# Optimization experiments

Hardware: AMD Instinct MI355X
Metric: run time of the kernel (lower is better)

## Reference

```python
import jax, jax.numpy as jnp
import numpy as np

LN_EPS = 1e-5


def _layer_norm(h, g, b):
    mu = jnp.mean(h, axis=-1, keepdims=True)
    var = jnp.mean((h - mu) ** 2, axis=-1, keepdims=True)
    return (h - mu) / jnp.sqrt(var + LN_EPS) * g + b


def setup_inputs() -> dict:
    key = jax.random.key(0)
    ks = jax.random.split(key, 12)
    B, N, D = 2, 2048, 768
    H, Dh = 12, 64
    Dp = D // 4  # 192, DynamicPositionBias width
    s = lambda fan_in: 1.0 / np.sqrt(fan_in)
    return {
        "x": jax.random.normal(ks[0], (B, N, D), jnp.float32),
        "qkv_w": jax.random.normal(ks[1], (D, 3 * H * Dh), jnp.float32) * s(D),
        "qkv_b": jax.random.normal(ks[2], (3 * H * Dh,), jnp.float32) * 0.02,
        "out_w": jax.random.normal(ks[3], (H * Dh, D), jnp.float32) * s(H * Dh),
        "out_b": jax.random.normal(ks[4], (D,), jnp.float32) * 0.02,
        "dpb_w_in": jax.random.normal(ks[5], (1, Dp), jnp.float32),
        "dpb_b_in": jax.random.normal(ks[6], (Dp,), jnp.float32) * 0.02,
        "dpb_w_hid": jax.random.normal(ks[7], (3, Dp, Dp), jnp.float32) * s(Dp),
        "dpb_b_hid": jax.random.normal(ks[8], (3, Dp), jnp.float32) * 0.02,
        "dpb_ln_g": jnp.ones((4, Dp), jnp.float32),
        "dpb_ln_b": jnp.zeros((4, Dp), jnp.float32),
        "dpb_w_out": jax.random.normal(ks[9], (Dp, 12), jnp.float32) * s(Dp),
        "dpb_b_out": jax.random.normal(ks[10], (12,), jnp.float32) * 0.02,
    }


def _dpb_bias(n, w_in, b_in, w_hid, b_hid, ln_g, ln_b, w_out, b_out):
    # positions -n+1 .. n-1, log-distance transform
    pos = jnp.arange(-n + 1, n, dtype=jnp.float32)[:, None]  # [2n-1, 1]
    pos = jnp.sign(pos) * jnp.log(jnp.abs(pos) + 1.0)
    h = jax.nn.silu(_layer_norm(pos @ w_in + b_in, ln_g[0], ln_b[0]))
    for l in range(3):
        h = jax.nn.silu(_layer_norm(h @ w_hid[l] + b_hid[l], ln_g[l + 1], ln_b[l + 1]))
    vals = h @ w_out + b_out  # [2n-1, H]
    idx = jnp.arange(n)[:, None] - jnp.arange(n)[None, :] + (n - 1)  # [n, n]
    bias = vals[idx]  # [n, n, H]
    return jnp.transpose(bias, (2, 0, 1))  # [H, n, n]


def reference(x, qkv_w, qkv_b, out_w, out_b,
              dpb_w_in, dpb_b_in, dpb_w_hid, dpb_b_hid,
              dpb_ln_g, dpb_ln_b, dpb_w_out, dpb_b_out):
    B, N, D = x.shape
    H = dpb_w_out.shape[-1]
    qkv = x @ qkv_w + qkv_b  # [B, N, 3*H*Dh]
    q, k, v = jnp.split(qkv, 3, axis=-1)
    split_heads = lambda t: jnp.transpose(t.reshape(B, N, H, -1), (0, 2, 1, 3))
    q, k, v = split_heads(q), split_heads(k), split_heads(v)  # [B, H, N, Dh]
    Dh = q.shape[-1]

    bias = _dpb_bias(N, dpb_w_in, dpb_b_in, dpb_w_hid, dpb_b_hid,
                     dpb_ln_g, dpb_ln_b, dpb_w_out, dpb_b_out)  # [H, N, N]

    scale = Dh ** -0.5
    sim = jnp.einsum("bhid,bhjd->bhij", q, k) * scale + bias[None]
    attn = jax.nn.softmax(sim, axis=-1)
    o = jnp.einsum("bhij,bhjd->bhid", attn, v)  # [B, H, N, Dh]
    o = jnp.transpose(o, (0, 2, 1, 3)).reshape(B, N, H * Dh)
    return o @ out_w + out_b
```

## Files before the change

### kernel.cpp

```cpp
#include <hip/hip_runtime.h>
#include <stdint.h>
#include <stddef.h>

typedef __bf16 bf16;
typedef __bf16 bf16x8 __attribute__((ext_vector_type(8)));
typedef float floatx4 __attribute__((ext_vector_type(4)));

typedef __attribute__((address_space(1))) void as1_void;
typedef __attribute__((address_space(3))) void as3_void;

__device__ __forceinline__ void async_ld16(const void* g, void* l) {
    __builtin_amdgcn_global_load_lds((as1_void*)g, (as3_void*)l, 16, 0, 0);
}

__device__ __forceinline__ floatx4 mfma16(bf16x8 a, bf16x8 b, floatx4 c) {
    return __builtin_amdgcn_mfma_f32_16x16x32_bf16(a, b, c, 0, 0, 0);
}

__device__ __forceinline__ unsigned cvtpk_bf16(float lo, float hi) {
    unsigned r;
    asm("v_cvt_pk_bf16_f32 %0, %1, %2" : "=v"(r) : "v"(lo), "v"(hi));
    return r;
}
__device__ __forceinline__ void pl32swap(unsigned &a, unsigned &b) {
    asm("v_permlane32_swap_b32 %0, %1" : "+v"(a), "+v"(b));
}
__device__ __forceinline__ void pl16swap(unsigned &a, unsigned &b) {
    asm("v_permlane16_swap_b32 %0, %1" : "+v"(a), "+v"(b));
}

#define LOG2E 1.4426950408889634f
#define SM_M2 24.0f
#define DP 192

__device__ __forceinline__ float ldsc(const void* p, size_t i, int isbf) {
    return isbf ? (float)((const bf16*)p)[i] : ((const float*)p)[i];
}
__device__ __forceinline__ bf16x8 ld8(const void* p, size_t i, int isbf) {
    if (isbf) return *(const bf16x8*)((const bf16*)p + i);
    const float* f = (const float*)p + i;
    float4 lo = *(const float4*)(f);
    float4 hi = *(const float4*)(f + 4);
    bf16x8 r;
    r[0]=(bf16)lo.x; r[1]=(bf16)lo.y; r[2]=(bf16)lo.z; r[3]=(bf16)lo.w;
    r[4]=(bf16)hi.x; r[5]=(bf16)hi.y; r[6]=(bf16)hi.z; r[7]=(bf16)hi.w;
    return r;
}
__device__ __forceinline__ int get_fl(const uint32_t* lng) {
    return (lng[0] == 0x3F803F80u) ? 1 : 0;
}

__device__ void transpose_body(const void* in, bf16* out, int R, int C,
                               int bx, int by, int fl, bf16 (*tile)[65]) {
    int c0 = bx * 64, r0 = by * 64;
    for (int i = threadIdx.x; i < 64*64; i += 256) {
        int rr = i >> 6, cc = i & 63;
        int gr = r0 + rr, gc = c0 + cc;
        tile[rr][cc] = (gr < R && gc < C)
                       ? (bf16)ldsc(in, (size_t)gr * C + gc, fl) : (bf16)0.0f;
    }
    __syncthreads();
    for (int i = threadIdx.x; i < 64*64; i += 256) {
        int rr = i >> 6, cc = i & 63;
        int oR = c0 + rr, oC = r0 + cc;
        if (oR < C && oC < R) out[(size_t)oR * R + oC] = tile[cc][rr];
    }
}

__global__ __launch_bounds__(256) void prep_kernel(
    const void* __restrict__ qkv_w, const void* __restrict__ out_w,
    bf16* __restrict__ wt_qkv, bf16* __restrict__ wt_out,
    const void* __restrict__ w_hid, const void* __restrict__ w_out,
    bf16* __restrict__ WtH, bf16* __restrict__ Wt12,
    const uint32_t* __restrict__ lngw,
    const void* __restrict__ x, bf16* __restrict__ xbf)
{
    __shared__ bf16 tile[64][65];
    const int fl = get_fl(lngw);
    const int bid = blockIdx.x;
    if (bid < 432) {
        transpose_body(qkv_w, wt_qkv, 768, 2304, bid % 36, bid / 36, fl, tile);
        return;
    }
    if (bid < 576) {
        int b2 = bid - 432;
        transpose_body(out_w, wt_out, 768, 768, b2 % 12, b2 / 12, fl, tile);
        return;
    }
    if (bid < 603) {
        transpose_body((const char*)0 + 0, nullptr, 0, 0, 0, 0, fl, tile);
        return;
    }
    if (bid < 606) {
        transpose_body(w_out, Wt12, 192, 12, 0, bid - 603, fl, tile);
        return;
    }
    size_t base = (size_t)(bid - 606) * 6144 + threadIdx.x * 8;
    #pragma unroll
    for (int c = 0; c < 3; c++)
        *(bf16x8*)(xbf + base + c*2048) = ld8(x, base + c*2048, fl);
}

__global__ __launch_bounds__(256) void prep_whid_kernel(
    const void* __restrict__ w_hid, bf16* __restrict__ WtH,
    const uint32_t* __restrict__ lngw)
{
    __shared__ bf16 tile[64][65];
    const int fl = get_fl(lngw);
    int l = blockIdx.x / 9, t9 = blockIdx.x % 9;
    transpose_body((const char*)w_hid + 0 + (size_t)l * DP * DP * (fl ? 2 : 4),
                   WtH + (size_t)l * DP * DP, DP, DP, t9 % 3, t9 / 3, fl, tile);
}

#define GK 768
#define HS 200

__global__ __launch_bounds__(256) void gemm0_dpb_kernel(
    const bf16* __restrict__ A, const bf16* __restrict__ Bt,
    const void* __restrict__ bias, const uint32_t* __restrict__ lngw,
    bf16* __restrict__ out0, bf16* __restrict__ out1, bf16* __restrict__ out2,
    const void* __restrict__ w_in, const void* __restrict__ b_in,
    const void* __restrict__ b_hid, const void* __restrict__ ln_g,
    const void* __restrict__ ln_b, const void* __restrict__ b_out,
    const bf16* __restrict__ WtH, const bf16* __restrict__ Wt12,
    float* __restrict__ vals_t)
{
    __shared__ __align__(16) char smem[16896];
    const int fl = get_fl(lngw);
    const int tid = threadIdx.x;
    const int wave = tid >> 6, lane = tid & 63;
    const int g = lane >> 4, cl = lane & 15;

    if (blockIdx.x >= 576) {
        bf16*  Hb   = (bf16*)smem;
        float* redS = (float*)(smem + 6400);
        float* redQ = (float*)(smem + 6656);
        const int pbase = (blockIdx.x - 576) * 16;

        float tpos[4];
        #pragma unroll
        for (int rg = 0; rg < 4; rg++) {
            int p = pbase + g*4 + rg;
            float pv = (float)p - 2047.0f;
            float sg = (pv > 0.0f) ? 1.0f : ((pv < 0.0f) ? -1.0f : 0.0f);
            tpos[rg] = sg * logf(fabsf(pv) + 1.0f);
        }
        int col[3];
        #pragma unroll
        for (int tt = 0; tt < 3; tt++) col[tt] = (wave*3 + tt)*16 + cl;

        floatx4 acc[3];
        #pragma unroll
        for (int tt = 0; tt < 3; tt++) {
            float wi = ldsc(w_in, col[tt], fl), bi = ldsc(b_in, col[tt], fl);
            #pragma unroll
            for (int rg = 0; rg < 4; rg++) acc[tt][rg] = tpos[rg]*wi + bi;
        }

        #pragma unroll 1
        for (int l = 0; l < 4; l++) {
            float s1[4], s2[4];
            #pragma unroll
            for (int rg = 0; rg < 4; rg++) {
                s1[rg] = acc[0][rg] + acc[1][rg] + acc[2][rg];
                s2[rg] = acc[0][rg]*acc[0][rg] + acc[1][rg]*acc[1][rg]
                       + acc[2][rg]*acc[2][rg];
            }
            #pragma unroll
            for (int m = 1; m <= 8; m <<= 1)
                #pragma unroll
                for (int rg = 0; rg < 4; rg++) {
                    s1[rg] += __shfl_xor(s1[rg], m);
                    s2[rg] += __shfl_xor(s2[rg], m);
                }
            if (cl == 0)
                #pragma unroll
                for (int rg = 0; rg < 4; rg++) {
                    redS[wave*16 + g*4 + rg] = s1[rg];
                    redQ[wave*16 + g*4 + rg] = s2[rg];
                }
            __syncthreads();
            float mu[4], rstd[4];
            #pragma unroll
            for (int rg = 0; rg < 4; rg++) {
                int row = g*4 + rg;
                float S = redS[row] + redS[16+row] + redS[32+row] + redS[48+row];
                float Q = redQ[row] + redQ[16+row] + redQ[32+row] + redQ[48+row];
                float m_ = S * (1.0f/DP);
                float v_ = Q * (1.0f/DP) - m_*m_;
                mu[rg] = m_;
                rstd[rg] = 1.0f / sqrtf(v_ + 1e-5f);
            }
            #pragma unroll
            for (int tt = 0; tt < 3; tt++) {
                float ga = ldsc(ln_g, l*DP + col[tt], fl);
                float be = ldsc(ln_b, l*DP + col[tt], fl);
                #pragma unroll
                for (int rg = 0; rg < 4; rg++) {
                    float y = (acc[tt][rg] - mu[rg]) * rstd[rg] * ga + be;
                    float sil = y / (1.0f + __expf(-y));
                    Hb[(g*4 + rg)*HS + col[tt]] = (bf16)sil;
                }
            }
            __syncthreads();
            if (l == 3) break;
            #pragma unroll
            for (int tt = 0; tt < 3; tt++) {
                float bh = ldsc(b_hid, l*DP + col[tt], fl);
                #pragma unroll
                for (int rg = 0; rg < 4; rg++) acc[tt][rg] = bh;
            }
            const bf16* Wl = WtH + (size_t)l * DP * DP;
            #pragma unroll
            for (int ks = 0; ks < 6; ks++) {
                bf16x8 af = *(const bf16x8*)(Hb + cl*HS + ks*32 + g*8);
                #pragma unroll
                for (int tt = 0; tt < 3; tt++) {
                    bf16x8 bfv = *(const bf16x8*)(Wl + (size_t)col[tt]*DP
                                                  + ks*32 + g*8);
                    acc[tt] = mfma16(af, bfv, acc[tt]);
                }
            }
        }
        if (wave == 0) {
            floatx4 facc = {};
            if (cl < 12) {
                float bo = ldsc(b_out, cl, fl);
                #pragma unroll
                for (int rg = 0; rg < 4; rg++) facc[rg] = bo;
            }
            #pragma unroll
            for (int ks = 0; ks < 6; ks++) {
                bf16x8 af = *(const bf16x8*)(Hb + cl*HS + ks*32 + g*8);
                bf16x8 bfv = {};
                if (cl < 12)
                    bfv = *(const bf16x8*)(Wt12 + (size_t)cl*DP + ks*32 + g*8);
                facc = mfma16(af, bfv, facc);
            }
            if (cl < 12)
                #pragma unroll
                for (int rg = 0; rg < 4; rg++) {
                    int p = pbase + g*4 + rg;
                    if (p < 4095) vals_t[cl*4095 + p] = facc[rg];
                }
        }
        return;
    }

    bf16* As = (bf16*)smem;
    bf16* Bs = (bf16*)(smem + 8192);
    const int tile = blockIdx.x;
    const int m0 = (tile / 18) * 128, n0 = (tile % 18) * 128;
    const int wm = (wave >> 1) * 64, wn = (wave & 1) * 64;

    const int e0 = wave*512 + lane*8;
    const int e1 = e0 + 2048;
    const int r0 = e0 >> 5, c0e = e0 & 31;
    const int r1 = e1 >> 5, c1e = e1 & 31;
    const bf16* Ag0 = A  + (size_t)(m0 + r0) * GK + c0e;
    const bf16* Ag1 = A  + (size_t)(m0 + r1) * GK + c1e;
    const bf16* Bg0 = Bt + (size_t)(n0 + r0) * GK + c0e;
    const bf16* Bg1 = Bt + (size_t)(n0 + r1) * GK + c1e;
    bf16* Al0 = As + e0;
    bf16* Al1 = As + e1;
    bf16* Bl0 = Bs + e0;
    bf16* Bl1 = Bs + e1;

    const int frow = lane & 15, fk = (lane >> 4) * 8;
    floatx4 acc[4][4] = {};

    for (int k0 = 0; k0 < GK; k0 += 32) {
        __syncthreads();
        async_ld16(Ag0 + k0, Al0);
        async_ld16(Ag1 + k0, Al1);
        async_ld16(Bg0 + k0, Bl0);
        async_ld16(Bg1 + k0, Bl1);
        __syncthreads();
        bf16x8 af[4], bfr[4];
        #pragma unroll
        for (int i = 0; i < 4; i++)
            af[i] = *(const bf16x8*)(As + (wm + i*16 + frow)*32 + fk);
        #pragma unroll
        for (int j = 0; j < 4; j++)
            bfr[j] = *(const bf16x8*)(Bs + (wn + j*16 + frow)*32 + fk);
        #pragma unroll
        for (int i = 0; i < 4; i++)
            #pragma unroll
            for (int j = 0; j < 4; j++)
                acc[i][j] = mfma16(af[i], bfr[j], acc[i][j]);
    }

    #pragma unroll
    for (int i = 0; i < 4; i++) {
        #pragma unroll
        for (int j = 0; j < 4; j++) {
            int Cc = n0 + wn + j*16 + cl;
            float bv = ldsc(bias, Cc, fl);
            #pragma unroll
            for (int rg = 0; rg < 4; rg++) {
                int R = m0 + wm + i*16 + g*4 + rg;
                float val = acc[i][j][rg] + bv;
                int which = Cc / 768;
                int c2 = Cc - which * 768;
                int hh = c2 >> 6, dd = c2 & 63;
                int bb = R >> 11, nn = R & 2047;
                if (which == 2) {
                    out2[(((size_t)(bb*12 + hh) * 64 + dd) * 2048) + nn]
                        = (bf16)val;
                } else {
                    bf16* dst = (which == 0) ? out0 : out1;
                    dst[((size_t)(bb*12 + hh) * 2048 + nn) * 64 + dd] = (bf16)val;
                }
            }
        }
    }
}

__global__ __launch_bounds__(256) void gemm_out(
    const bf16* __restrict__ A, const bf16* __restrict__ Bt,
    const void* __restrict__ bias, const uint32_t* __restrict__ lngw,
    void* __restrict__ out0)
{
    __shared__ __align__(16) bf16 As[128*32];
    __shared__ __align__(16) bf16 Bs[128*32];
    const int fl  = get_fl(lngw);
    const int tid = threadIdx.x;
    const int wave = tid >> 6, lane = tid & 63;
    const int m0 = blockIdx.y * 128, n0 = blockIdx.x * 128;
    const int wm = (wave >> 1) * 64, wn = (wave & 1) * 64;

    const int e0 = wave*512 + lane*8;
    const int e1 = e0 + 2048;
    const int r0 = e0 >> 5, c0e = e0 & 31;
    const int r1 = e1 >> 5, c1e = e1 & 31;
    const bf16* Ag0 = A  + (size_t)(m0 + r0) * GK + c0e;
    const bf16* Ag1 = A  + (size_t)(m0 + r1) * GK + c1e;
    const bf16* Bg0 = Bt + (size_t)(n0 + r0) * GK + c0e;
    const bf16* Bg1 = Bt + (size_t)(n0 + r1) * GK + c1e;
    bf16* Al0 = As + e0;
    bf16* Al1 = As + e1;
    bf16* Bl0 = Bs + e0;
    bf16* Bl1 = Bs + e1;

    const int frow = lane & 15, fk = (lane >> 4) * 8;
    floatx4 acc[4][4] = {};

    for (int k0 = 0; k0 < GK; k0 += 32) {
        __syncthreads();
        async_ld16(Ag0 + k0, Al0);
        async_ld16(Ag1 + k0, Al1);
        async_ld16(Bg0 + k0, Bl0);
        async_ld16(Bg1 + k0, Bl1);
        __syncthreads();
        bf16x8 af[4], bfr[4];
        #pragma unroll
        for (int i = 0; i < 4; i++)
            af[i] = *(const bf16x8*)(As + (wm + i*16 + frow)*32 + fk);
        #pragma unroll
        for (int j = 0; j < 4; j++)
            bfr[j] = *(const bf16x8*)(Bs + (wn + j*16 + frow)*32 + fk);
        #pragma unroll
        for (int i = 0; i < 4; i++)
            #pragma unroll
            for (int j = 0; j < 4; j++)
                acc[i][j] = mfma16(af[i], bfr[j], acc[i][j]);
    }

    const int g = lane >> 4, cl = lane & 15;
    #pragma unroll
    for (int i = 0; i < 4; i++) {
        #pragma unroll
        for (int j = 0; j < 4; j++) {
            int Cc = n0 + wn + j*16 + cl;
            float bv = ldsc(bias, Cc, fl);
            #pragma unroll
            for (int rg = 0; rg < 4; rg++) {
                int R = m0 + wm + i*16 + g*4 + rg;
                float val = acc[i][j][rg] + bv;
                size_t oi = (size_t)R * 768 + Cc;
                if (fl) ((bf16*)out0)[oi]  = (bf16)val;
                else    ((float*)out0)[oi] = val;
            }
        }
    }
}

__global__ __launch_bounds__(256) void attn_kernel(
    const bf16* __restrict__ qws, const bf16* __restrict__ kws,
    const bf16* __restrict__ vwst, const float* __restrict__ vals_t,
    bf16* __restrict__ ows)
{
    __shared__ __align__(16) bf16 Qs[64*72];
    __shared__ __align__(16) bf16 Ks[64*72];
    __shared__ __align__(16) bf16 Vt[64*72];
    __shared__ float bias_s[128];

    const int tid = threadIdx.x;
    const int wave = tid >> 6, lane = tid & 63;
    const int g = lane >> 4, cl = lane & 15;
    const int q0 = blockIdx.x * 64;
    const int h = blockIdx.y, b = blockIdx.z;
    const size_t bh = (size_t)(b*12 + h);
    const bf16* qp  = qws  + bh * 2048 * 64;
    const bf16* kp  = kws  + bh * 2048 * 64;
    const bf16* vpt = vwst + bh * 64 * 2048;
    const float* vrow = vals_t + h * 4095;

    for (int i = tid; i < 512; i += 256) {
        int r = i >> 3, c = (i & 7) * 8;
        *(bf16x8*)(Qs + r*72 + c) = *(const bf16x8*)(qp + (size_t)(q0 + r)*64 + c);
    }
    __syncthreads();
    bf16x8 aq0 = *(const bf16x8*)(Qs + (wave*16 + cl)*72 + g*8);
    bf16x8 aq1 = *(const bf16x8*)(Qs + (wave*16 + cl)*72 + 32 + g*8);

    const int sr0 = tid >> 3, sc0 = (tid & 7) * 8;
    const int sr1 = sr0 + 32;

    bf16x8 kreg0 = *(const bf16x8*)(kp + (size_t)sr0 * 64 + sc0);
    bf16x8 kreg1 = *(const bf16x8*)(kp + (size_t)sr1 * 64 + sc0);
    bf16x8 vreg0 = *(const bf16x8*)(vpt + (size_t)sr0 * 2048 + sc0);
    bf16x8 vreg1 = *(const bf16x8*)(vpt + (size_t)sr1 * 2048 + sc0);
    float  breg  = 0.0f;
    if (tid < 127) breg = vrow[q0 + 1984 + tid];

    floatx4 accO[4] = {};
    float lsum = 0.0f;
    const int il_b = wave*16 + g*4;
    const float c1 = 0.125f * LOG2E;
    const int bbase = wave*16 + cl - 4*g + 63;

    for (int jv0 = 0; jv0 < 2048; jv0 += 64) {
        __syncthreads();
        *(bf16x8*)(Ks + sr0*72 + sc0) = kreg0;
        *(bf16x8*)(Ks + sr1*72 + sc0) = kreg1;
        *(bf16x8*)(Vt + sr0*72 + sc0) = vreg0;
        *(bf16x8*)(Vt + sr1*72 + sc0) = vreg1;
        if (tid < 127) bias_s[tid] = breg * LOG2E - SM_M2;
        __syncthreads();

        if (jv0 + 64 < 2048) {
            const int nj = jv0 + 64;
            kreg0 = *(const bf16x8*)(kp + (size_t)(nj + sr0) * 64 + sc0);
            kreg1 = *(const bf16x8*)(kp + (size_t)(nj + sr1) * 64 + sc0);
            vreg0 = *(const bf16x8*)(vpt + (size_t)sr0 * 2048 + nj + sc0);
            vreg1 = *(const bf16x8*)(vpt + (size_t)sr1 * 2048 + nj + sc0);
            if (tid < 127) breg = vrow[q0 - nj + 1984 + tid];
        }

        floatx4 accS[4];
        #pragma unroll
        for (int jt = 0; jt < 4; jt++) {
            bf16x8 ak0 = *(const bf16x8*)(Ks + (jt*16 + cl)*72 + g*8);
            bf16x8 ak1 = *(const bf16x8*)(Ks + (jt*16 + cl)*72 + 32 + g*8);
            floatx4 z = {};
            z = mfma16(ak0, aq0, z);
            z = mfma16(ak1, aq1, z);
            accS[jt] = z;
        }

        unsigned pk[4][2];
        #pragma unroll
        for (int jt = 0; jt < 4; jt++) {
            float pv[4];
            #pragma unroll
            for (int rg = 0; rg < 4; rg++) {
                float x2 = fmaf(accS[jt][rg], c1, bias_s[bbase - jt*16 - rg]);
                x2 = fminf(x2, 80.0f);
                pv[rg] = __builtin_amdgcn_exp2f(x2);
            }
            lsum += (pv[0] + pv[1]) + (pv[2] + pv[3]);
            pk[jt][0] = cvtpk_bf16(pv[0], pv[1]);
            pk[jt][1] = cvtpk_bf16(pv[2], pv[3]);
        }

        bf16x8 ap[2];
        #pragma unroll
        for (int kst = 0; kst < 2; kst++) {
            unsigned e0p = pk[2*kst][0], f0p = pk[2*kst+1][0];
            unsigned e1p = pk[2*kst][1], f1p = pk[2*kst+1][1];
            pl32swap(e0p, f0p);
            pl16swap(e0p, f0p);
            pl32swap(e1p, f1p);
            pl16swap(e1p, f1p);
            union { unsigned u[4]; bf16x8 v; } uu;
            uu.u[0] = e0p; uu.u[1] = e1p; uu.u[2] = f0p; uu.u[3] = f1p;
            ap[kst] = uu.v;
        }

        #pragma unroll
        for (int dt = 0; dt < 4; dt++) {
            #pragma unroll
            for (int kst = 0; kst < 2; kst++) {
                bf16x8 bv = *(const bf16x8*)(Vt + (dt*16 + cl)*72 + kst*32 + g*8);
                accO[dt] = mfma16(ap[kst], bv, accO[dt]);
            }
        }
    }

    lsum += __shfl_xor(lsum, 16);
    lsum += __shfl_xor(lsum, 32);

    #pragma unroll
    for (int rg = 0; rg < 4; rg++) {
        float l = __shfl(lsum, g*4 + rg);
        float inv = 1.0f / l;
        size_t row = (size_t)(b*2048 + q0 + il_b + rg) * 768 + h*64;
        #pragma unroll
        for (int dt = 0; dt < 4; dt++)
            ows[row + dt*16 + cl] = (bf16)(accO[dt][rg] * inv);
    }
}

extern "C" void kernel_launch(void* const* d_in, const int* in_sizes, int n_in,
                              void* d_out, int out_size, void* d_ws, size_t ws_size,
                              hipStream_t stream)
{
    (void)in_sizes; (void)n_in; (void)out_size;
    const void* x     = d_in[0];
    const void* qkv_w = d_in[1];
    const void* qkv_b = d_in[2];
    const void* out_w = d_in[3];
    const void* out_b = d_in[4];
    const void* w_in  = d_in[5];
    const void* b_in  = d_in[6];
    const void* w_hid = d_in[7];
    const void* b_hid = d_in[8];
    const void* ln_g  = d_in[9];
    const void* ln_b  = d_in[10];
    const void* w_out = d_in[11];
    const void* b_out = d_in[12];

    const size_t NEED = 4915200 + 4ull*6291456;
    if (ws_size < NEED) return;

    char* ws = (char*)d_ws;
    float* vals_t = (float*)(ws);
    bf16*  wt_qkv = (bf16*)(ws + 196608);
    bf16*  wt_out = (bf16*)(ws + 196608 + 3538944);
    bf16*  q_ws   = (bf16*)(ws + 4915200);
    bf16*  k_ws   = (bf16*)(ws + 4915200 + 6291456);
    bf16*  v_wst  = (bf16*)(ws + 4915200 + 2*6291456);
    bf16*  o_ws   = (bf16*)(ws + 4915200 + 3*6291456);
    bf16*  x_bf   = o_ws;
    bf16*  WtH    = (bf16*)d_out;
    bf16*  Wt12   = WtH + 3*DP*DP;

    prep_kernel<<<1118, 256, 0, stream>>>(qkv_w, out_w, wt_qkv, wt_out,
                                          w_hid, w_out, WtH, Wt12,
                                          (const uint32_t*)ln_g, x, x_bf);
    prep_whid_kernel<<<27, 256, 0, stream>>>(w_hid, WtH, (const uint32_t*)ln_g);
    gemm0_dpb_kernel<<<832, 256, 0, stream>>>(
        x_bf, wt_qkv, qkv_b, (const uint32_t*)ln_g, q_ws, k_ws, v_wst,
        w_in, b_in, b_hid, ln_g, ln_b, b_out, WtH, Wt12, vals_t);
    attn_kernel<<<dim3(32, 12, 2), 256, 0, stream>>>(q_ws, k_ws, v_wst,
                                                     vals_t, o_ws);
    gemm_out<<<dim3(6, 32), 256, 0, stream>>>(o_ws, wt_out, out_b,
                                              (const uint32_t*)ln_g, d_out);
}
```

Measured before the change: 218.7 us.

## Double-buffer attention K/V tiles, XCD-aware block remapping, fold w_hid transpose into prep

Attention now double-buffers K, V and bias tiles in LDS, cutting the two barriers per iteration to one and prefetching two tiles ahead in registers. Both the QKV GEMM and attention remap the linear block index so that consecutive blocks on the same XCD (blockIdx & 7) share rows or a (batch, head) pair, aiming at better L2 reuse. The separate w_hid transpose launch is folded into previously idle blocks of the prep kernel, removing one launch. The cost is roughly double the attention LDS footprint, which may lower occupancy.

```diff
diff --git a/kernel.cpp b/kernel.cpp
--- a/kernel.cpp
+++ b/kernel.cpp
@@ -88,7 +88,10 @@
         return;
     }
     if (bid < 603) {
-        transpose_body((const char*)0 + 0, nullptr, 0, 0, 0, 0, fl, tile);
+        int b2 = bid - 576, l = b2 / 9, t9 = b2 % 9;
+        transpose_body((const char*)w_hid + (size_t)l * DP * DP * (fl ? 2 : 4),
+                       WtH + (size_t)l * DP * DP, DP, DP, t9 % 3, t9 / 3,
+                       fl, tile);
         return;
     }
     if (bid < 606) {
@@ -99,17 +102,6 @@
     #pragma unroll
     for (int c = 0; c < 3; c++)
         *(bf16x8*)(xbf + base + c*2048) = ld8(x, base + c*2048, fl);
-}
-
-__global__ __launch_bounds__(256) void prep_whid_kernel(
-    const void* __restrict__ w_hid, bf16* __restrict__ WtH,
-    const uint32_t* __restrict__ lngw)
-{
-    __shared__ bf16 tile[64][65];
-    const int fl = get_fl(lngw);
-    int l = blockIdx.x / 9, t9 = blockIdx.x % 9;
-    transpose_body((const char*)w_hid + 0 + (size_t)l * DP * DP * (fl ? 2 : 4),
-                   WtH + (size_t)l * DP * DP, DP, DP, t9 % 3, t9 / 3, fl, tile);
 }
 
 #define GK 768
@@ -249,8 +241,8 @@
 
     bf16* As = (bf16*)smem;
     bf16* Bs = (bf16*)(smem + 8192);
-    const int tile = blockIdx.x;
-    const int m0 = (tile / 18) * 128, n0 = (tile % 18) * 128;
+    const int xcd8 = blockIdx.x & 7, slot = blockIdx.x >> 3;
+    const int m0 = (xcd8*4 + slot/18) * 128, n0 = (slot % 18) * 128;
     const int wm = (wave >> 1) * 64, wn = (wave & 1) * 64;
 
     const int e0 = wave*512 + lane*8;
@@ -391,16 +383,18 @@
     bf16* __restrict__ ows)
 {
     __shared__ __align__(16) bf16 Qs[64*72];
-    __shared__ __align__(16) bf16 Ks[64*72];
-    __shared__ __align__(16) bf16 Vt[64*72];
-    __shared__ float bias_s[128];
+    __shared__ __align__(16) bf16 Ks[2][64*72];
+    __shared__ __align__(16) bf16 Vt[2][64*72];
+    __shared__ float bias_s[2][128];
 
     const int tid = threadIdx.x;
     const int wave = tid >> 6, lane = tid & 63;
     const int g = lane >> 4, cl = lane & 15;
-    const int q0 = blockIdx.x * 64;
-    const int h = blockIdx.y, b = blockIdx.z;
-    const size_t bh = (size_t)(b*12 + h);
+    const int xcd8 = blockIdx.x & 7, slot = blockIdx.x >> 3;
+    const int bh_ = xcd8*3 + (slot >> 5);
+    const int q0 = (slot & 31) * 64;
+    const int h = bh_ % 12, b = bh_ / 12;
+    const size_t bh = (size_t)bh_;
     const bf16* qp  = qws  + bh * 2048 * 64;
     const bf16* kp  = kws  + bh * 2048 * 64;
     const bf16* vpt = vwst + bh * 64 * 2048;
@@ -410,9 +404,6 @@
         int r = i >> 3, c = (i & 7) * 8;
         *(bf16x8*)(Qs + r*72 + c) = *(const bf16x8*)(qp + (size_t)(q0 + r)*64 + c);
     }
-    __syncthreads();
-    bf16x8 aq0 = *(const bf16x8*)(Qs + (wave*16 + cl)*72 + g*8);
-    bf16x8 aq1 = *(const bf16x8*)(Qs + (wave*16 + cl)*72 + 32 + g*8);
 
     const int sr0 = tid >> 3, sc0 = (tid & 7) * 8;
     const int sr1 = sr0 + 32;
@@ -423,6 +414,21 @@
     bf16x8 vreg1 = *(const bf16x8*)(vpt + (size_t)sr1 * 2048 + sc0);
     float  breg  = 0.0f;
     if (tid < 127) breg = vrow[q0 + 1984 + tid];
+    *(bf16x8*)(Ks[0] + sr0*72 + sc0) = kreg0;
+    *(bf16x8*)(Ks[0] + sr1*72 + sc0) = kreg1;
+    *(bf16x8*)(Vt[0] + sr0*72 + sc0) = vreg0;
+    *(bf16x8*)(Vt[0] + sr1*72 + sc0) = vreg1;
+    if (tid < 127) bias_s[0][tid] = breg * LOG2E - SM_M2;
+
+    kreg0 = *(const bf16x8*)(kp + (size_t)(64 + sr0) * 64 + sc0);
+    kreg1 = *(const bf16x8*)(kp + (size_t)(64 + sr1) * 64 + sc0);
+    vreg0 = *(const bf16x8*)(vpt + (size_t)sr0 * 2048 + 64 + sc0);
+    vreg1 = *(const bf16x8*)(vpt + (size_t)sr1 * 2048 + 64 + sc0);
+    if (tid < 127) breg = vrow[q0 - 64 + 1984 + tid];
+
+    __syncthreads();
+    bf16x8 aq0 = *(const bf16x8*)(Qs + (wave*16 + cl)*72 + g*8);
+    bf16x8 aq1 = *(const bf16x8*)(Qs + (wave*16 + cl)*72 + 32 + g*8);
 
     floatx4 accO[4] = {};
     float lsum = 0.0f;
@@ -430,17 +436,19 @@
     const float c1 = 0.125f * LOG2E;
     const int bbase = wave*16 + cl - 4*g + 63;
 
-    for (int jv0 = 0; jv0 < 2048; jv0 += 64) {
-        __syncthreads();
-        *(bf16x8*)(Ks + sr0*72 + sc0) = kreg0;
-        *(bf16x8*)(Ks + sr1*72 + sc0) = kreg1;
-        *(bf16x8*)(Vt + sr0*72 + sc0) = vreg0;
-        *(bf16x8*)(Vt + sr1*72 + sc0) = vreg1;
-        if (tid < 127) bias_s[tid] = breg * LOG2E - SM_M2;
-        __syncthreads();
-
-        if (jv0 + 64 < 2048) {
-            const int nj = jv0 + 64;
+    for (int j = 0; j < 32; ++j) {
+        const int cur = j & 1;
+        if (j + 1 < 32) {
+            bf16* Kn = Ks[cur ^ 1];
+            bf16* Vn = Vt[cur ^ 1];
+            *(bf16x8*)(Kn + sr0*72 + sc0) = kreg0;
+            *(bf16x8*)(Kn + sr1*72 + sc0) = kreg1;
+            *(bf16x8*)(Vn + sr0*72 + sc0) = vreg0;
+            *(bf16x8*)(Vn + sr1*72 + sc0) = vreg1;
+            if (tid < 127) bias_s[cur ^ 1][tid] = breg * LOG2E - SM_M2;
+        }
+        if (j + 2 < 32) {
+            const int nj = (j + 2) * 64;
             kreg0 = *(const bf16x8*)(kp + (size_t)(nj + sr0) * 64 + sc0);
             kreg1 = *(const bf16x8*)(kp + (size_t)(nj + sr1) * 64 + sc0);
             vreg0 = *(const bf16x8*)(vpt + (size_t)sr0 * 2048 + nj + sc0);
@@ -448,11 +456,15 @@
             if (tid < 127) breg = vrow[q0 - nj + 1984 + tid];
         }
 
+        const bf16* Kc = Ks[cur];
+        const bf16* Vc = Vt[cur];
+        const float* bs = bias_s[cur];
+
         floatx4 accS[4];
         #pragma unroll
         for (int jt = 0; jt < 4; jt++) {
-            bf16x8 ak0 = *(const bf16x8*)(Ks + (jt*16 + cl)*72 + g*8);
-            bf16x8 ak1 = *(const bf16x8*)(Ks + (jt*16 + cl)*72 + 32 + g*8);
+            bf16x8 ak0 = *(const bf16x8*)(Kc + (jt*16 + cl)*72 + g*8);
+            bf16x8 ak1 = *(const bf16x8*)(Kc + (jt*16 + cl)*72 + 32 + g*8);
             floatx4 z = {};
             z = mfma16(ak0, aq0, z);
             z = mfma16(ak1, aq1, z);
@@ -465,7 +477,7 @@
             float pv[4];
             #pragma unroll
             for (int rg = 0; rg < 4; rg++) {
-                float x2 = fmaf(accS[jt][rg], c1, bias_s[bbase - jt*16 - rg]);
+                float x2 = fmaf(accS[jt][rg], c1, bs[bbase - jt*16 - rg]);
                 x2 = fminf(x2, 80.0f);
                 pv[rg] = __builtin_amdgcn_exp2f(x2);
             }
@@ -492,10 +504,12 @@
         for (int dt = 0; dt < 4; dt++) {
             #pragma unroll
             for (int kst = 0; kst < 2; kst++) {
-                bf16x8 bv = *(const bf16x8*)(Vt + (dt*16 + cl)*72 + kst*32 + g*8);
+                bf16x8 bv = *(const bf16x8*)(Vc + (dt*16 + cl)*72 + kst*32 + g*8);
                 accO[dt] = mfma16(ap[kst], bv, accO[dt]);
             }
         }
+
+        __syncthreads();
     }
 
     lsum += __shfl_xor(lsum, 16);
@@ -549,12 +563,10 @@
     prep_kernel<<<1118, 256, 0, stream>>>(qkv_w, out_w, wt_qkv, wt_out,
                                           w_hid, w_out, WtH, Wt12,
                                           (const uint32_t*)ln_g, x, x_bf);
-    prep_whid_kernel<<<27, 256, 0, stream>>>(w_hid, WtH, (const uint32_t*)ln_g);
     gemm0_dpb_kernel<<<832, 256, 0, stream>>>(
         x_bf, wt_qkv, qkv_b, (const uint32_t*)ln_g, q_ws, k_ws, v_wst,
         w_in, b_in, b_hid, ln_g, ln_b, b_out, WtH, Wt12, vals_t);
-    attn_kernel<<<dim3(32, 12, 2), 256, 0, stream>>>(q_ws, k_ws, v_wst,
-                                                     vals_t, o_ws);
+    attn_kernel<<<768, 256, 0, stream>>>(q_ws, k_ws, v_wst, vals_t, o_ws);
     gemm_out<<<dim3(6, 32), 256, 0, stream>>>(o_ws, wt_out, out_b,
                                               (const uint32_t*)ln_g, d_out);
 }
```

New measurement: 209.0 us. 4.4% less time.
